# Optimization experiments

Hardware: AMD Instinct MI355X
Metric: run time of the kernel (lower is better)

## Reference

```python
import jax, jax.numpy as jnp
import numpy as np

B, Q, K, H, DV = 16, 256, 256, 256, 256


def setup_inputs() -> dict:
    key = jax.random.key(0)
    ks = jax.random.split(key, 6)
    return {
        "queries": jax.random.normal(ks[0], (B, Q, H), dtype=jnp.float32),
        "keys": jax.random.normal(ks[1], (B, K, H), dtype=jnp.float32),
        "values": jax.random.normal(ks[2], (B, K, DV), dtype=jnp.float32),
        "W_q": jax.random.normal(ks[3], (H, H), dtype=jnp.float32) / np.sqrt(H),
        "W_k": jax.random.normal(ks[4], (H, H), dtype=jnp.float32) / np.sqrt(H),
        "w_v": jax.random.normal(ks[5], (H,), dtype=jnp.float32) / np.sqrt(H),
    }


def reference(queries, keys, values, W_q, W_k, w_v):
    # Linear projections (nn.Linear: x @ W.T), bias-free
    q = jnp.einsum("bqd,hd->bqh", queries, W_q)  # [B,Q,H]
    k = jnp.einsum("bkd,hd->bkh", keys, W_k)      # [B,K,H]
    # Broadcast add -> tanh -> scalar projection
    features = jnp.tanh(q[:, :, None, :] + k[:, None, :, :])  # [B,Q,K,H]
    scores = jnp.einsum("bqkh,h->bqk", features, w_v)          # [B,Q,K]
    attn = jax.nn.softmax(scores, axis=-1)                      # [B,Q,K]
    return jnp.einsum("bqk,bkv->bqv", attn, values)            # [B,Q,DV]
```

## Files before the change

### kernel.cpp

```cpp
#include <hip/hip_runtime.h>
#include <hip/hip_fp16.h>

#define Bn 16
#define Qn 256
#define Kn 256
#define Hn 256
#define DVn 256

constexpr float C2    = 2.8853900817779268f;
constexpr float LOG2E = 1.4426950408889634f;

typedef __attribute__((ext_vector_type(8))) short bf16x8;
typedef __attribute__((ext_vector_type(4))) float f32x4;

__device__ __forceinline__ float fast_exp2(float x) { return __builtin_amdgcn_exp2f(x); }
__device__ __forceinline__ float fast_rcp(float x)  { return __builtin_amdgcn_rcpf(x); }

__device__ __forceinline__ unsigned short f2bf(float x) {
    unsigned u = __float_as_uint(x);
    u += 0x7fffu + ((u >> 16) & 1u);
    return (unsigned short)(u >> 16);
}

__global__ __launch_bounds__(256)
void prep_kernel(const float* __restrict__ q, const float* __restrict__ kx,
                 const float* __restrict__ wq, const float* __restrict__ wk,
                 const float* __restrict__ V,
                 unsigned short* __restrict__ Xb, unsigned short* __restrict__ Wb,
                 float* __restrict__ Vp)
{
    const int g = blockIdx.x * 256 + threadIdx.x;
    {
        const float* xs = (g < 131072) ? (q + (size_t)g * 8)
                                       : (kx + (size_t)(g - 131072) * 8);
        float4 x0 = *(const float4*)xs;
        float4 x1 = *(const float4*)(xs + 4);
        ushort4 o0, o1;
        o0.x = f2bf(x0.x); o0.y = f2bf(x0.y); o0.z = f2bf(x0.z); o0.w = f2bf(x0.w);
        o1.x = f2bf(x1.x); o1.y = f2bf(x1.y); o1.z = f2bf(x1.z); o1.w = f2bf(x1.w);
        *(ushort4*)(Xb + (size_t)g * 8)     = o0;
        *(ushort4*)(Xb + (size_t)g * 8 + 4) = o1;
    }
    if (g < 32768) {
        const float* ws = (g < 16384) ? (wq + (size_t)g * 4)
                                      : (wk + (size_t)(g - 16384) * 4);
        float4 w0 = *(const float4*)ws;
        ushort4 o;
        o.x = f2bf(w0.x); o.y = f2bf(w0.y); o.z = f2bf(w0.z); o.w = f2bf(w0.w);
        *(ushort4*)(Wb + (size_t)g * 4) = o;
    }
    {
        const int p   = g;
        const int bk4 = p >> 8, dv = p & 255;
        const int b   = bk4 >> 6, k4 = bk4 & 63;
        const float* src = V + ((size_t)(b * Kn + 4 * k4)) * DVn + dv;
        float4 o;
        o.x = src[0 * DVn]; o.y = src[1 * DVn]; o.z = src[2 * DVn]; o.w = src[3 * DVn];
        *(float4*)(Vp + (size_t)p * 4) = o;
    }
}

__global__ __launch_bounds__(256)
void proj_mfma_kernel(const unsigned short* __restrict__ Xb,
                      const unsigned short* __restrict__ Wb,
                      float* __restrict__ Eq, unsigned short* __restrict__ Ekb)
{
    const int tid  = threadIdx.x;
    const int wvid = tid >> 6, lane = tid & 63;
    const int m0   = blockIdx.x * 16;
    const int n0   = wvid * 64;
    const bool isQ = (m0 < 4096);
    const int r16  = lane & 15, q8 = (lane >> 4) * 8;

    const unsigned short* Xrow  = Xb + (size_t)(m0 + r16) * 256 + q8;
    const unsigned short* Wbase = Wb + (isQ ? 0 : 65536);

    bf16x8 afr[8];
    #pragma unroll
    for (int s = 0; s < 8; ++s) afr[s] = *(const bf16x8*)(Xrow + s * 32);

    f32x4 acc[4];
    #pragma unroll
    for (int nt = 0; nt < 4; ++nt) {
        const unsigned short* Wrow = Wbase + (size_t)(n0 + nt * 16 + r16) * 256 + q8;
        f32x4 c = {0.f, 0.f, 0.f, 0.f};
        #pragma unroll
        for (int s = 0; s < 8; ++s) {
            bf16x8 bfr = *(const bf16x8*)(Wrow + s * 32);
            c = __builtin_amdgcn_mfma_f32_16x16x32_bf16(afr[s], bfr, c, 0, 0, 0);
        }
        acc[nt] = c;
    }
    const int rbase = (lane >> 4) * 4;
    #pragma unroll
    for (int nt = 0; nt < 4; ++nt) {
        const int n = n0 + nt * 16 + r16;
        #pragma unroll
        for (int r = 0; r < 4; ++r) {
            const int m = m0 + rbase + r;
            const float val = fast_exp2(C2 * acc[nt][r]);
            if (isQ) {
                Eq[(size_t)m * 256 + n] = val;
            } else {
                const int kr = m - 4096, b = kr >> 8, kk = kr & 255;
                Ekb[(((size_t)(b * 64 + (n >> 2))) * 256 + kk) * 4 + (n & 3)] = f2bf(val);
            }
        }
    }
}

__global__ __launch_bounds__(256)
void fused_attn_kernel(const float* __restrict__ Eq, const unsigned short* __restrict__ Ekb,
                       const float* __restrict__ wv, const float* __restrict__ Vp,
                       float* __restrict__ out)
{
    const int b  = blockIdx.y;
    const int q0 = blockIdx.x * 4;
    __shared__ __align__(16) float sPv[256 * 4];
    __shared__ float sredM[4][4];
    __shared__ float sredS[4][4];
    const int tid = threadIdx.x;

    const float* eq0 = Eq + (size_t)(b * Qn + q0) * Hn;

    float sc[4] = {0.f, 0.f, 0.f, 0.f};
    const uint2* ekp = (const uint2*)Ekb + (size_t)b * 16384 + tid;
    uint2 e[4];
    #pragma unroll
    for (int g = 0; g < 4; ++g) e[g] = ekp[g * 256];
    for (int it = 0; it < 16; ++it) {
        uint2 en[4];
        if (it < 15) {
            #pragma unroll
            for (int g = 0; g < 4; ++g) en[g] = ekp[(4 * (it + 1) + g) * 256];
        }
        const int h0 = it * 16;
        float ek[16];
        #pragma unroll
        for (int g = 0; g < 4; ++g) {
            ek[4*g+0] = __uint_as_float(e[g].x << 16);
            ek[4*g+1] = __uint_as_float(e[g].x & 0xFFFF0000u);
            ek[4*g+2] = __uint_as_float(e[g].y << 16);
            ek[4*g+3] = __uint_as_float(e[g].y & 0xFFFF0000u);
        }
        #pragma unroll
        for (int g = 0; g < 4; ++g) {
            const float4 wa = *(const float4*)(wv + h0 + 4 * g);
            #pragma unroll
            for (int qq = 0; qq < 4; ++qq) {
                const float4 ea = *(const float4*)(eq0 + qq * 256 + h0 + 4 * g);
                float a = sc[qq];
                a = fmaf(wa.x, fast_rcp(fmaf(ea.x, ek[4*g+0], 1.f)), a);
                a = fmaf(wa.y, fast_rcp(fmaf(ea.y, ek[4*g+1], 1.f)), a);
                a = fmaf(wa.z, fast_rcp(fmaf(ea.z, ek[4*g+2], 1.f)), a);
                a = fmaf(wa.w, fast_rcp(fmaf(ea.w, ek[4*g+3], 1.f)), a);
                sc[qq] = a;
            }
        }
        #pragma unroll
        for (int g = 0; g < 4; ++g) e[g] = en[g];
    }

    const int w = tid >> 6, lane = tid & 63;
    #pragma unroll
    for (int qq = 0; qq < 4; ++qq) {
        sc[qq] = -2.0f * sc[qq];
        float mx = sc[qq];
        #pragma unroll
        for (int off = 32; off; off >>= 1) mx = fmaxf(mx, __shfl_xor(mx, off, 64));
        if (lane == 0) sredM[qq][w] = mx;
    }
    __syncthreads();
    float pq[4];
    #pragma unroll
    for (int qq = 0; qq < 4; ++qq) {
        const float mx = fmaxf(fmaxf(sredM[qq][0], sredM[qq][1]),
                               fmaxf(sredM[qq][2], sredM[qq][3]));
        pq[qq] = fast_exp2(LOG2E * (sc[qq] - mx));
        float s = pq[qq];
        #pragma unroll
        for (int off = 32; off; off >>= 1) s += __shfl_xor(s, off, 64);
        if (lane == 0) sredS[qq][w] = s;
    }
    *(float4*)&sPv[tid * 4] = make_float4(pq[0], pq[1], pq[2], pq[3]);
    __syncthreads();
    float rinv[4];
    #pragma unroll
    for (int qq = 0; qq < 4; ++qq)
        rinv[qq] = fast_rcp(sredS[qq][0] + sredS[qq][1] + sredS[qq][2] + sredS[qq][3]);

    float acc[4] = {0.f, 0.f, 0.f, 0.f};
    const float4* vp = (const float4*)Vp + (size_t)b * 64 * 256 + tid;
    float4 vv = vp[0];
    for (int k4 = 0; k4 < 64; ++k4) {
        float4 vn;
        if (k4 < 63) vn = vp[(k4 + 1) * 256];
        const float vj[4] = {vv.x, vv.y, vv.z, vv.w};
        #pragma unroll
        for (int j = 0; j < 4; ++j) {
            const float4 p4 = *(const float4*)&sPv[(4 * k4 + j) * 4];
            acc[0] = fmaf(p4.x, vj[j], acc[0]);
            acc[1] = fmaf(p4.y, vj[j], acc[1]);
            acc[2] = fmaf(p4.z, vj[j], acc[2]);
            acc[3] = fmaf(p4.w, vj[j], acc[3]);
        }
        vv = vn;
    }
    float* ob = out + (size_t)(b * Qn + q0) * DVn + tid;
    ob[0 * DVn] = acc[0] * rinv[0];
    ob[1 * DVn] = acc[1] * rinv[1];
    ob[2 * DVn] = acc[2] * rinv[2];
    ob[3 * DVn] = acc[3] * rinv[3];
}

extern "C" void kernel_launch(void* const* d_in, const int* in_sizes, int n_in,
                              void* d_out, int out_size, void* d_ws, size_t ws_size,
                              hipStream_t stream) {
    const float* queries = (const float*)d_in[0];
    const float* keys    = (const float*)d_in[1];
    const float* values  = (const float*)d_in[2];
    const float* W_q     = (const float*)d_in[3];
    const float* W_k     = (const float*)d_in[4];
    const float* w_v     = (const float*)d_in[5];
    float* out = (float*)d_out;

    float*          Eq  = (float*)d_ws;
    unsigned short* Ekb = (unsigned short*)(Eq + (size_t)Bn * Qn * Hn);
    float*          Vp  = (float*)(Ekb + (size_t)Bn * Kn * Hn);
    unsigned short* Xb  = (unsigned short*)(Vp + (size_t)Bn * Kn * DVn);
    unsigned short* Wb  = Xb + (size_t)2 * Bn * Qn * Hn;

    prep_kernel<<<dim3(1024), 256, 0, stream>>>(queries, keys, W_q, W_k, values,
                                                Xb, Wb, Vp);
    proj_mfma_kernel<<<dim3(512), 256, 0, stream>>>(Xb, Wb, Eq, Ekb);
    fused_attn_kernel<<<dim3(64, 16), 256, 0, stream>>>(Eq, Ekb, w_v, Vp, out);
}
```

Measured before the change: 128.9 us.

## Fuse bf16 conversion into projection kernel and split attention H/K across block halves

Removes the separate prep kernel by converting fp32 inputs and weights to bf16 on the fly inside the MFMA projection kernel, which also takes over the V repacking. The projection grid doubles, with each block covering half the N columns. The attention kernel now uses 512 threads. The two halves split the H reduction for scores and the K reduction for P·V, and partial sums are combined through shared memory. This cuts one launch and the bf16 intermediate round-trip and raises parallelism per block, but weights are now re-read and re-converted redundantly and extra barriers are added.

Result: slower. 132.8 us (+3.0%).

```diff
diff --git a/kernel.cpp b/kernel.cpp
--- a/kernel.cpp
+++ b/kernel.cpp
@@ -1,5 +1,4 @@
 #include <hip/hip_runtime.h>
-#include <hip/hip_fp16.h>
 
 #define Bn 16
 #define Qn 256
@@ -22,78 +21,54 @@
     return (unsigned short)(u >> 16);
 }
 
+__device__ __forceinline__ bf16x8 cvt8(const float* p) {
+    float4 x0 = *(const float4*)p;
+    float4 x1 = *(const float4*)(p + 4);
+    bf16x8 r;
+    r[0] = (short)f2bf(x0.x); r[1] = (short)f2bf(x0.y);
+    r[2] = (short)f2bf(x0.z); r[3] = (short)f2bf(x0.w);
+    r[4] = (short)f2bf(x1.x); r[5] = (short)f2bf(x1.y);
+    r[6] = (short)f2bf(x1.z); r[7] = (short)f2bf(x1.w);
+    return r;
+}
+
 __global__ __launch_bounds__(256)
-void prep_kernel(const float* __restrict__ q, const float* __restrict__ kx,
-                 const float* __restrict__ wq, const float* __restrict__ wk,
-                 const float* __restrict__ V,
-                 unsigned short* __restrict__ Xb, unsigned short* __restrict__ Wb,
-                 float* __restrict__ Vp)
-{
-    const int g = blockIdx.x * 256 + threadIdx.x;
-    {
-        const float* xs = (g < 131072) ? (q + (size_t)g * 8)
-                                       : (kx + (size_t)(g - 131072) * 8);
-        float4 x0 = *(const float4*)xs;
-        float4 x1 = *(const float4*)(xs + 4);
-        ushort4 o0, o1;
-        o0.x = f2bf(x0.x); o0.y = f2bf(x0.y); o0.z = f2bf(x0.z); o0.w = f2bf(x0.w);
-        o1.x = f2bf(x1.x); o1.y = f2bf(x1.y); o1.z = f2bf(x1.z); o1.w = f2bf(x1.w);
-        *(ushort4*)(Xb + (size_t)g * 8)     = o0;
-        *(ushort4*)(Xb + (size_t)g * 8 + 4) = o1;
-    }
-    if (g < 32768) {
-        const float* ws = (g < 16384) ? (wq + (size_t)g * 4)
-                                      : (wk + (size_t)(g - 16384) * 4);
-        float4 w0 = *(const float4*)ws;
-        ushort4 o;
-        o.x = f2bf(w0.x); o.y = f2bf(w0.y); o.z = f2bf(w0.z); o.w = f2bf(w0.w);
-        *(ushort4*)(Wb + (size_t)g * 4) = o;
-    }
-    {
-        const int p   = g;
-        const int bk4 = p >> 8, dv = p & 255;
-        const int b   = bk4 >> 6, k4 = bk4 & 63;
-        const float* src = V + ((size_t)(b * Kn + 4 * k4)) * DVn + dv;
-        float4 o;
-        o.x = src[0 * DVn]; o.y = src[1 * DVn]; o.z = src[2 * DVn]; o.w = src[3 * DVn];
-        *(float4*)(Vp + (size_t)p * 4) = o;
-    }
-}
-
-__global__ __launch_bounds__(256)
-void proj_mfma_kernel(const unsigned short* __restrict__ Xb,
-                      const unsigned short* __restrict__ Wb,
-                      float* __restrict__ Eq, unsigned short* __restrict__ Ekb)
+void proj_mfma_kernel(const float* __restrict__ q, const float* __restrict__ kx,
+                      const float* __restrict__ wq, const float* __restrict__ wk,
+                      const float* __restrict__ V,
+                      float* __restrict__ Eq, unsigned short* __restrict__ Ekb,
+                      float* __restrict__ Vp)
 {
     const int tid  = threadIdx.x;
     const int wvid = tid >> 6, lane = tid & 63;
-    const int m0   = blockIdx.x * 16;
-    const int n0   = wvid * 64;
+    const int bid  = blockIdx.x;
+    const int m0   = (bid >> 1) * 16;
+    const int n0   = (bid & 1) * 128 + wvid * 32;
     const bool isQ = (m0 < 4096);
     const int r16  = lane & 15, q8 = (lane >> 4) * 8;
 
-    const unsigned short* Xrow  = Xb + (size_t)(m0 + r16) * 256 + q8;
-    const unsigned short* Wbase = Wb + (isQ ? 0 : 65536);
-
+    const float* Xrow = (isQ ? q + (size_t)(m0 + r16) * 256
+                             : kx + (size_t)(m0 - 4096 + r16) * 256) + q8;
     bf16x8 afr[8];
     #pragma unroll
-    for (int s = 0; s < 8; ++s) afr[s] = *(const bf16x8*)(Xrow + s * 32);
-
-    f32x4 acc[4];
-    #pragma unroll
-    for (int nt = 0; nt < 4; ++nt) {
-        const unsigned short* Wrow = Wbase + (size_t)(n0 + nt * 16 + r16) * 256 + q8;
+    for (int s = 0; s < 8; ++s) afr[s] = cvt8(Xrow + s * 32);
+
+    const float* Wbase = isQ ? wq : wk;
+    f32x4 acc[2];
+    #pragma unroll
+    for (int nt = 0; nt < 2; ++nt) {
+        const float* Wrow = Wbase + (size_t)(n0 + nt * 16 + r16) * 256 + q8;
         f32x4 c = {0.f, 0.f, 0.f, 0.f};
         #pragma unroll
         for (int s = 0; s < 8; ++s) {
-            bf16x8 bfr = *(const bf16x8*)(Wrow + s * 32);
+            bf16x8 bfr = cvt8(Wrow + s * 32);
             c = __builtin_amdgcn_mfma_f32_16x16x32_bf16(afr[s], bfr, c, 0, 0, 0);
         }
         acc[nt] = c;
     }
     const int rbase = (lane >> 4) * 4;
     #pragma unroll
-    for (int nt = 0; nt < 4; ++nt) {
+    for (int nt = 0; nt < 2; ++nt) {
         const int n = n0 + nt * 16 + r16;
         #pragma unroll
         for (int r = 0; r < 4; ++r) {
@@ -107,30 +82,45 @@
             }
         }
     }
-}
-
-__global__ __launch_bounds__(256)
+    {
+        const int p   = bid * 256 + tid;
+        const int bk4 = p >> 8, dv = p & 255;
+        const int b   = bk4 >> 6, k4 = bk4 & 63;
+        const float* src = V + ((size_t)(b * Kn + 4 * k4)) * DVn + dv;
+        float4 o;
+        o.x = src[0 * DVn]; o.y = src[1 * DVn]; o.z = src[2 * DVn]; o.w = src[3 * DVn];
+        *(float4*)(Vp + (size_t)p * 4) = o;
+    }
+}
+
+__global__ __launch_bounds__(512, 8)
 void fused_attn_kernel(const float* __restrict__ Eq, const unsigned short* __restrict__ Ekb,
                        const float* __restrict__ wv, const float* __restrict__ Vp,
                        float* __restrict__ out)
 {
-    const int b  = blockIdx.y;
-    const int q0 = blockIdx.x * 4;
+    const int b    = blockIdx.y;
+    const int q0   = blockIdx.x * 4;
+    const int tid  = threadIdx.x;
+    const int kk   = tid & 255;
+    const int half = tid >> 8;
+    const int halfu = __builtin_amdgcn_readfirstlane(half);
+
+    __shared__ __align__(16) float sPart[2][256][4];
     __shared__ __align__(16) float sPv[256 * 4];
-    __shared__ float sredM[4][4];
-    __shared__ float sredS[4][4];
-    const int tid = threadIdx.x;
-
-    const float* eq0 = Eq + (size_t)(b * Qn + q0) * Hn;
+    __shared__ float sredM[4][8];
+    __shared__ float sredS[4][8];
+
+    const float* eq0 = Eq + (size_t)(b * Qn + q0) * Hn + halfu * 128;
+    const float* wv0 = wv + halfu * 128;
 
     float sc[4] = {0.f, 0.f, 0.f, 0.f};
-    const uint2* ekp = (const uint2*)Ekb + (size_t)b * 16384 + tid;
+    const uint2* ekp = (const uint2*)Ekb + (size_t)b * 16384 + (size_t)(halfu * 32) * 256 + kk;
     uint2 e[4];
     #pragma unroll
     for (int g = 0; g < 4; ++g) e[g] = ekp[g * 256];
-    for (int it = 0; it < 16; ++it) {
+    for (int it = 0; it < 8; ++it) {
         uint2 en[4];
-        if (it < 15) {
+        if (it < 7) {
             #pragma unroll
             for (int g = 0; g < 4; ++g) en[g] = ekp[(4 * (it + 1) + g) * 256];
         }
@@ -145,7 +135,7 @@
         }
         #pragma unroll
         for (int g = 0; g < 4; ++g) {
-            const float4 wa = *(const float4*)(wv + h0 + 4 * g);
+            const float4 wa = *(const float4*)(wv0 + h0 + 4 * g);
             #pragma unroll
             for (int qq = 0; qq < 4; ++qq) {
                 const float4 ea = *(const float4*)(eq0 + qq * 256 + h0 + 4 * g);
@@ -161,11 +151,17 @@
         for (int g = 0; g < 4; ++g) e[g] = en[g];
     }
 
+    *(float4*)&sPart[half][kk][0] = make_float4(sc[0], sc[1], sc[2], sc[3]);
+    __syncthreads();
+    const float4 pa = *(const float4*)&sPart[0][kk][0];
+    const float4 pb = *(const float4*)&sPart[1][kk][0];
+    float tot[4] = {pa.x + pb.x, pa.y + pb.y, pa.z + pb.z, pa.w + pb.w};
+
     const int w = tid >> 6, lane = tid & 63;
     #pragma unroll
     for (int qq = 0; qq < 4; ++qq) {
-        sc[qq] = -2.0f * sc[qq];
-        float mx = sc[qq];
+        tot[qq] = -2.0f * tot[qq];
+        float mx = tot[qq];
         #pragma unroll
         for (int off = 32; off; off >>= 1) mx = fmaxf(mx, __shfl_xor(mx, off, 64));
         if (lane == 0) sredM[qq][w] = mx;
@@ -174,31 +170,37 @@
     float pq[4];
     #pragma unroll
     for (int qq = 0; qq < 4; ++qq) {
-        const float mx = fmaxf(fmaxf(sredM[qq][0], sredM[qq][1]),
-                               fmaxf(sredM[qq][2], sredM[qq][3]));
-        pq[qq] = fast_exp2(LOG2E * (sc[qq] - mx));
+        float mx = sredM[qq][0];
+        #pragma unroll
+        for (int i = 1; i < 8; ++i) mx = fmaxf(mx, sredM[qq][i]);
+        pq[qq] = fast_exp2(LOG2E * (tot[qq] - mx));
         float s = pq[qq];
         #pragma unroll
         for (int off = 32; off; off >>= 1) s += __shfl_xor(s, off, 64);
         if (lane == 0) sredS[qq][w] = s;
     }
-    *(float4*)&sPv[tid * 4] = make_float4(pq[0], pq[1], pq[2], pq[3]);
+    if (halfu == 0) *(float4*)&sPv[kk * 4] = make_float4(pq[0], pq[1], pq[2], pq[3]);
     __syncthreads();
     float rinv[4];
     #pragma unroll
-    for (int qq = 0; qq < 4; ++qq)
-        rinv[qq] = fast_rcp(sredS[qq][0] + sredS[qq][1] + sredS[qq][2] + sredS[qq][3]);
+    for (int qq = 0; qq < 4; ++qq) {
+        float s = sredS[qq][0];
+        #pragma unroll
+        for (int i = 1; i < 8; ++i) s += sredS[qq][i];
+        rinv[qq] = fast_rcp(0.5f * s);
+    }
 
     float acc[4] = {0.f, 0.f, 0.f, 0.f};
-    const float4* vp = (const float4*)Vp + (size_t)b * 64 * 256 + tid;
+    const float4* vp = (const float4*)Vp + (size_t)b * 64 * 256 + (size_t)(halfu * 32) * 256 + kk;
     float4 vv = vp[0];
-    for (int k4 = 0; k4 < 64; ++k4) {
+    for (int k4 = 0; k4 < 32; ++k4) {
         float4 vn;
-        if (k4 < 63) vn = vp[(k4 + 1) * 256];
+        if (k4 < 31) vn = vp[(k4 + 1) * 256];
+        const int kb = (halfu * 32 + k4) * 4;
         const float vj[4] = {vv.x, vv.y, vv.z, vv.w};
         #pragma unroll
         for (int j = 0; j < 4; ++j) {
-            const float4 p4 = *(const float4*)&sPv[(4 * k4 + j) * 4];
+            const float4 p4 = *(const float4*)&sPv[(kb + j) * 4];
             acc[0] = fmaf(p4.x, vj[j], acc[0]);
             acc[1] = fmaf(p4.y, vj[j], acc[1]);
             acc[2] = fmaf(p4.z, vj[j], acc[2]);
@@ -206,11 +208,19 @@
         }
         vv = vn;
     }
-    float* ob = out + (size_t)(b * Qn + q0) * DVn + tid;
-    ob[0 * DVn] = acc[0] * rinv[0];
-    ob[1 * DVn] = acc[1] * rinv[1];
-    ob[2 * DVn] = acc[2] * rinv[2];
-    ob[3 * DVn] = acc[3] * rinv[3];
+    *(float4*)&sPart[half][kk][0] = make_float4(acc[0], acc[1], acc[2], acc[3]);
+    __syncthreads();
+    {
+        const int dv = kk;
+        const float4 u0 = *(const float4*)&sPart[0][dv][0];
+        const float4 u1 = *(const float4*)&sPart[1][dv][0];
+        float a0, a1;
+        if (halfu == 0) { a0 = u0.x + u1.x; a1 = u0.y + u1.y; }
+        else            { a0 = u0.z + u1.z; a1 = u0.w + u1.w; }
+        float* ob = out + (size_t)(b * Qn + q0 + 2 * halfu) * DVn + dv;
+        ob[0]   = a0 * rinv[2 * halfu + 0];
+        ob[DVn] = a1 * rinv[2 * halfu + 1];
+    }
 }
 
 extern "C" void kernel_launch(void* const* d_in, const int* in_sizes, int n_in,
@@ -227,11 +237,8 @@
     float*          Eq  = (float*)d_ws;
     unsigned short* Ekb = (unsigned short*)(Eq + (size_t)Bn * Qn * Hn);
     float*          Vp  = (float*)(Ekb + (size_t)Bn * Kn * Hn);
-    unsigned short* Xb  = (unsigned short*)(Vp + (size_t)Bn * Kn * DVn);
-    unsigned short* Wb  = Xb + (size_t)2 * Bn * Qn * Hn;
-
-    prep_kernel<<<dim3(1024), 256, 0, stream>>>(queries, keys, W_q, W_k, values,
-                                                Xb, Wb, Vp);
-    proj_mfma_kernel<<<dim3(512), 256, 0, stream>>>(Xb, Wb, Eq, Ekb);
-    fused_attn_kernel<<<dim3(64, 16), 256, 0, stream>>>(Eq, Ekb, w_v, Vp, out);
-}
+
+    proj_mfma_kernel<<<dim3(1024), 256, 0, stream>>>(queries, keys, W_q, W_k, values,
+                                                     Eq, Ekb, Vp);
+    fused_attn_kernel<<<dim3(64, 16), 512, 0, stream>>>(Eq, Ekb, w_v, Vp, out);
+}
```
